# Kernel optimization log

Hardware: AMD Instinct MI355X
Metric: run time of the kernel (lower is better)

## Reference

```python
import jax, jax.numpy as jnp
import numpy as np

N = 100000      # nodes
E = 1600000     # edges
F_IN = 128      # in_feat
H = 128         # hidden_dim
C = 40          # num_class


def setup_inputs() -> dict:
    key = jax.random.key(0)
    ks = jax.random.split(key, 4)
    x = jax.random.normal(ks[0], (N, F_IN), dtype=jnp.float32)
    edge_index = jax.random.randint(ks[1], (2, E), 0, N, dtype=jnp.int32)
    # glorot-ish init for the two GCN layers
    W1 = jax.random.normal(ks[2], (F_IN, H), dtype=jnp.float32) * (1.0 / np.sqrt(F_IN))
    b1 = jnp.zeros((H,), dtype=jnp.float32)
    W2 = jax.random.normal(ks[3], (H, C), dtype=jnp.float32) * (1.0 / np.sqrt(H))
    b2 = jnp.zeros((C,), dtype=jnp.float32)
    return {"x": x, "edge_index": edge_index, "W1": W1, "b1": b1, "W2": W2, "b2": b2}


def _gcn_conv(x, W, b, row, col, norm, n_nodes):
    # GCNConv: linear transform, then normalized sum-aggregation over edges, + bias
    h = x @ W                                  # [N, d_out]
    msg = h[row] * norm[:, None]               # gather sources, scale  [E', d_out]
    out = jax.ops.segment_sum(msg, col, num_segments=n_nodes)  # scatter-add to targets
    return out + b


def reference(x, edge_index, W1, b1, W2, b2):
    n_nodes = x.shape[0]
    # add self-loops (PyG GCNConv default)
    loops = jnp.arange(n_nodes, dtype=edge_index.dtype)
    row = jnp.concatenate([edge_index[0], loops])  # sources
    col = jnp.concatenate([edge_index[1], loops])  # targets
    # symmetric normalization: deg computed at targets with unit edge weights
    deg = jax.ops.segment_sum(jnp.ones_like(col, dtype=x.dtype), col, num_segments=n_nodes)
    dis = jnp.where(deg > 0, jax.lax.rsqrt(jnp.maximum(deg, 1e-12)), 0.0)
    norm = dis[row] * dis[col]                 # [E+N]

    h = jax.nn.relu(_gcn_conv(x, W1, b1, row, col, norm, n_nodes))
    out = _gcn_conv(h, W2, b2, row, col, norm, n_nodes)
    return out
```

## Files before the change

kernel.cpp:

```cpp
#include <hip/hip_runtime.h>
#include <hip/hip_bf16.h>


#define FB_SHIFT 9

__device__ __forceinline__ unsigned bf16rn(float f) {
    unsigned x = __float_as_uint(f);
    unsigned r = ((x >> 16) & 1u) + 0x7fffu;
    return (x + r) >> 16;
}
__device__ __forceinline__ float bf_lo(unsigned u) { return __uint_as_float(u << 16); }
__device__ __forceinline__ float bf_hi(unsigned u) { return __uint_as_float(u & 0xffff0000u); }

typedef __bf16 bf16x8 __attribute__((ext_vector_type(8)));
typedef float  f32x4  __attribute__((ext_vector_type(4)));

__global__ __launch_bounds__(512) void k_bcount(const int* __restrict__ col,
                                                int* __restrict__ btot, int E) {
    __shared__ int h[256];
    const int tid = threadIdx.x;
    if (tid < 256) h[tid] = 0;
    __syncthreads();
    const int base = blockIdx.x * 4096;
#pragma unroll
    for (int k = 0; k < 8; ++k) {
        int e = base + k * 512 + tid;
        if (e < E) atomicAdd(&h[col[e] >> FB_SHIFT], 1);
    }
    __syncthreads();
    if (tid < 256) {
        int v = h[tid];
        if (v > 0) atomicAdd(&btot[tid], v);
    }
}

__global__ __launch_bounds__(256) void k_bscan(const int* __restrict__ btot,
                                               int* __restrict__ bbase,
                                               int* __restrict__ bcur) {
    __shared__ int s[256];
    const int t = threadIdx.x;
    int v = btot[t];
    s[t] = v;
    __syncthreads();
#pragma unroll
    for (int off = 1; off < 256; off <<= 1) {
        int u = (t >= off) ? s[t - off] : 0;
        __syncthreads();
        s[t] += u;
        __syncthreads();
    }
    int excl = s[t] - v;
    bbase[t] = excl;
    bcur[t] = excl;
    if (t == 255) bbase[256] = s[255];
}

__global__ __launch_bounds__(512) void k_binfill(const int* __restrict__ row,
                                                 const int* __restrict__ col,
                                                 int* __restrict__ bcur,
                                                 unsigned* __restrict__ bins, int E) {
    __shared__ int hist[256];
    __shared__ int scn[256];
    __shared__ int gbase[256];
    __shared__ int rcnt[256];
    __shared__ unsigned stage[4096];
    __shared__ unsigned char bkts[4096];

    const int tid = threadIdx.x;
    const int base = blockIdx.x * 4096;

    if (tid < 256) { hist[tid] = 0; rcnt[tid] = 0; }
    __syncthreads();

    unsigned mypk[8];
    int      myb[8];
#pragma unroll
    for (int k = 0; k < 8; ++k) {
        int e = base + k * 512 + tid;
        if (e < E) {
            int r = row[e], c = col[e];
            int b = c >> FB_SHIFT;
            mypk[k] = ((unsigned)r << FB_SHIFT) | (unsigned)(c & ((1 << FB_SHIFT) - 1));
            myb[k] = b;
            atomicAdd(&hist[b], 1);
        } else {
            myb[k] = -1;
        }
    }
    __syncthreads();

    int v = 0;
    if (tid < 256) { v = hist[tid]; scn[tid] = v; }
    __syncthreads();
#pragma unroll
    for (int off = 1; off < 256; off <<= 1) {
        int t = (tid >= off && tid < 256) ? scn[tid - off] : 0;
        __syncthreads();
        if (tid < 256) scn[tid] += t;
        __syncthreads();
    }
    if (tid < 256) {
        int excl = scn[tid] - v;
        scn[tid] = excl;
    }
    __syncthreads();

#pragma unroll
    for (int k = 0; k < 8; ++k) {
        int b = myb[k];
        if (b >= 0) {
            int slot = scn[b] + atomicAdd(&rcnt[b], 1);
            stage[slot] = mypk[k];
            bkts[slot] = (unsigned char)b;
        }
    }

    if (tid < 256 && hist[tid] > 0) gbase[tid] = atomicAdd(&bcur[tid], hist[tid]);
    __syncthreads();

    int total = scn[255] + hist[255];
    for (int s = tid; s < total; s += 512) {
        unsigned u = stage[s];
        int b = bkts[s];
        bins[gbase[b] + (s - scn[b])] = u;
    }
}

__global__ __launch_bounds__(1024) void k_fill2(const unsigned* __restrict__ bins,
                                                const int* __restrict__ bbase,
                                                int* __restrict__ rowptr,
                                                float* __restrict__ dis,
                                                int* __restrict__ pair, int N) {
    __shared__ int cnt[512];
    __shared__ int lcur[512];
    __shared__ int ssum[256];
    const int tid = threadIdx.x;
    const int b = blockIdx.x;
    const int n0 = b << FB_SHIFT;
    const int start = bbase[b];
    const int end = bbase[b + 1];

    if (tid < 512) cnt[tid] = 0;
    __syncthreads();

    for (int i = start + tid; i < end; i += 1024)
        atomicAdd(&cnt[bins[i] & ((1 << FB_SHIFT) - 1)], 1);
    __syncthreads();

    int c0 = 0, c1 = 0, vsum = 0;
    if (tid < 256) {
        c0 = cnt[2 * tid]; c1 = cnt[2 * tid + 1];
        vsum = c0 + c1;
        ssum[tid] = vsum;
    }
    __syncthreads();
#pragma unroll
    for (int off = 1; off < 256; off <<= 1) {
        int u = (tid >= off && tid < 256) ? ssum[tid - off] : 0;
        __syncthreads();
        if (tid < 256) ssum[tid] += u;
        __syncthreads();
    }
    if (tid < 256) {
        int e0 = start + ssum[tid] - vsum;
        int e1 = e0 + c0;
        lcur[2 * tid] = e0;
        lcur[2 * tid + 1] = e1;
        int node0 = n0 + 2 * tid;
        int node1 = node0 + 1;
        if (node0 <= N) rowptr[node0] = e0;
        if (node1 <= N) rowptr[node1] = e1;
        if (node0 < N) dis[node0] = rsqrtf((float)(c0 + 1));
        if (node1 < N) dis[node1] = rsqrtf((float)(c1 + 1));
    }
    __syncthreads();

    for (int i = start + tid; i < end; i += 1024) {
        unsigned u = bins[i];
        int pos = atomicAdd(&lcur[u & ((1 << FB_SHIFT) - 1)], 1);
        pair[pos] = (int)(u >> FB_SHIFT);
    }
}

__global__ __launch_bounds__(256) void k_cvtall(const float* __restrict__ x,
                                                const float* __restrict__ dis,
                                                unsigned* __restrict__ xb,
                                                const float* __restrict__ W1,
                                                const float* __restrict__ W2,
                                                unsigned* __restrict__ Wt,
                                                unsigned* __restrict__ W2t, int n32) {
    int i = blockIdx.x * 256 + threadIdx.x;
    if (i < n32) {
        float4 v = ((const float4*)x)[i];
        float d = dis[i >> 5];
        uint2 o;
        o.x = bf16rn(v.x * d) | (bf16rn(v.y * d) << 16);
        o.y = bf16rn(v.z * d) | (bf16rn(v.w * d) << 16);
        ((uint2*)xb)[i] = o;
        return;
    }
    int t = i - n32;
    if (t < 8192) {
        int n = t >> 6, kk = (t & 63) * 2;
        unsigned lo = bf16rn(W1[(size_t)kk * 128 + n]);
        unsigned hi = bf16rn(W1[(size_t)(kk + 1) * 128 + n]);
        Wt[t] = lo | (hi << 16);
    } else if (t < 8192 + 3072) {
        int u = t - 8192;
        int n = u >> 6, kk = (u & 63) * 2;
        unsigned lo = 0, hi = 0;
        if (n < 40) {
            lo = bf16rn(W2[(size_t)kk * 40 + n]);
            hi = bf16rn(W2[(size_t)(kk + 1) * 40 + n]);
        }
        W2t[u] = lo | (hi << 16);
    }
}

__global__ __launch_bounds__(256) void k_gather1(const unsigned* __restrict__ xb,
                                                 const int* __restrict__ rowptr,
                                                 const int* __restrict__ pair,
                                                 const float* __restrict__ dis,
                                                 unsigned* __restrict__ xab, int N) {
    int gw = (blockIdx.x * 256 + threadIdx.x) >> 6;
    int lane = threadIdx.x & 63;
    if (gw >= N) return;
    float dv = dis[gw];
    unsigned us = xb[(size_t)gw * 64 + lane];
    float2 acc = make_float2(bf_lo(us), bf_hi(us));
    int j = rowptr[gw], je = rowptr[gw + 1];

    for (; j + 7 < je; j += 8) {
        int r0 = pair[j],     r1 = pair[j + 1], r2 = pair[j + 2], r3 = pair[j + 3];
        int r4 = pair[j + 4], r5 = pair[j + 5], r6 = pair[j + 6], r7 = pair[j + 7];
        unsigned a0 = xb[(size_t)r0 * 64 + lane];
        unsigned a1 = xb[(size_t)r1 * 64 + lane];
        unsigned a2 = xb[(size_t)r2 * 64 + lane];
        unsigned a3 = xb[(size_t)r3 * 64 + lane];
        unsigned a4 = xb[(size_t)r4 * 64 + lane];
        unsigned a5 = xb[(size_t)r5 * 64 + lane];
        unsigned a6 = xb[(size_t)r6 * 64 + lane];
        unsigned a7 = xb[(size_t)r7 * 64 + lane];
        acc.x += bf_lo(a0); acc.y += bf_hi(a0);
        acc.x += bf_lo(a1); acc.y += bf_hi(a1);
        acc.x += bf_lo(a2); acc.y += bf_hi(a2);
        acc.x += bf_lo(a3); acc.y += bf_hi(a3);
        acc.x += bf_lo(a4); acc.y += bf_hi(a4);
        acc.x += bf_lo(a5); acc.y += bf_hi(a5);
        acc.x += bf_lo(a6); acc.y += bf_hi(a6);
        acc.x += bf_lo(a7); acc.y += bf_hi(a7);
    }
    for (; j + 3 < je; j += 4) {
        int r0 = pair[j], r1 = pair[j + 1], r2 = pair[j + 2], r3 = pair[j + 3];
        unsigned a0 = xb[(size_t)r0 * 64 + lane];
        unsigned a1 = xb[(size_t)r1 * 64 + lane];
        unsigned a2 = xb[(size_t)r2 * 64 + lane];
        unsigned a3 = xb[(size_t)r3 * 64 + lane];
        acc.x += bf_lo(a0); acc.y += bf_hi(a0);
        acc.x += bf_lo(a1); acc.y += bf_hi(a1);
        acc.x += bf_lo(a2); acc.y += bf_hi(a2);
        acc.x += bf_lo(a3); acc.y += bf_hi(a3);
    }
    for (; j < je; ++j) {
        unsigned a0 = xb[(size_t)pair[j] * 64 + lane];
        acc.x += bf_lo(a0); acc.y += bf_hi(a0);
    }
    xab[(size_t)gw * 64 + lane] = bf16rn(dv * acc.x) | (bf16rn(dv * acc.y) << 16);
}

__global__ __launch_bounds__(256) void k_gemm12(const unsigned* __restrict__ Ab,
                                                const unsigned* __restrict__ Wt,
                                                const unsigned* __restrict__ W2t,
                                                const float* __restrict__ bias,
                                                const float* __restrict__ dis,
                                                unsigned* __restrict__ Zb, int M) {
    __shared__ char smem[70144];
    char* Abase = smem;
    char* Bbase = smem + 34816;
    float* ldis = (float*)(smem + 69632);

    const int tid = threadIdx.x;
    const int r0 = blockIdx.x * 128;

#pragma unroll
    for (int s = 0; s < 8; ++s) {
        int l = tid + s * 256;
        int row = l >> 4, q = l & 15;
        uint4 va = *(const uint4*)(Ab + (size_t)(r0 + row) * 64 + q * 4);
        *(uint4*)(Abase + row * 272 + q * 16) = va;
        uint4 vb = *(const uint4*)(Wt + (size_t)row * 64 + q * 4);
        *(uint4*)(Bbase + row * 272 + q * 16) = vb;
    }
    if (tid < 128) {
        int rr = r0 + tid;
        ldis[tid] = (rr < M) ? dis[rr] : 0.f;
    }
    __syncthreads();

    const int wv = tid >> 6, lane = tid & 63;
    const int quad = lane >> 4, mcol = lane & 15;

    f32x4 acc1[2][8];
#pragma unroll
    for (int rt = 0; rt < 2; ++rt)
#pragma unroll
        for (int ct = 0; ct < 8; ++ct) acc1[rt][ct] = (f32x4){0.f, 0.f, 0.f, 0.f};

#pragma unroll
    for (int ks = 0; ks < 4; ++ks) {
        bf16x8 a[2], b[8];
#pragma unroll
        for (int rt = 0; rt < 2; ++rt) {
            int row = wv * 32 + rt * 16 + mcol;
            a[rt] = *(const bf16x8*)(Abase + row * 272 + ks * 64 + quad * 16);
        }
#pragma unroll
        for (int ct = 0; ct < 8; ++ct) {
            int n = ct * 16 + mcol;
            b[ct] = *(const bf16x8*)(Bbase + n * 272 + ks * 64 + quad * 16);
        }
#pragma unroll
        for (int rt = 0; rt < 2; ++rt)
#pragma unroll
            for (int ct = 0; ct < 8; ++ct)
                acc1[rt][ct] = __builtin_amdgcn_mfma_f32_16x16x32_bf16(
                    a[rt], b[ct], acc1[rt][ct], 0, 0, 0);
    }
    __syncthreads();

    unsigned short* Hs = (unsigned short*)Bbase;
#pragma unroll
    for (int rt = 0; rt < 2; ++rt)
#pragma unroll
        for (int ct = 0; ct < 8; ++ct) {
            float bb = bias[ct * 16 + mcol];
#pragma unroll
            for (int r = 0; r < 4; ++r) {
                float v = acc1[rt][ct][r] + bb;
                v = v > 0.f ? v : 0.f;
                int orow = wv * 32 + rt * 16 + quad * 4 + r;
                Hs[orow * 136 + ct * 16 + mcol] = (unsigned short)bf16rn(v);
            }
        }
#pragma unroll
    for (int s = 0; s < 3; ++s) {
        int l = tid + s * 256;
        int row = l >> 4, q = l & 15;
        uint4 vb = *(const uint4*)(W2t + (size_t)row * 64 + q * 4);
        *(uint4*)(Abase + row * 272 + q * 16) = vb;
    }
    __syncthreads();

    f32x4 acc2[2][3];
#pragma unroll
    for (int rt = 0; rt < 2; ++rt)
#pragma unroll
        for (int ct = 0; ct < 3; ++ct) acc2[rt][ct] = (f32x4){0.f, 0.f, 0.f, 0.f};

#pragma unroll
    for (int ks = 0; ks < 4; ++ks) {
        bf16x8 a[2], b[3];
#pragma unroll
        for (int rt = 0; rt < 2; ++rt) {
            int row = wv * 32 + rt * 16 + mcol;
            a[rt] = *(const bf16x8*)(Bbase + row * 272 + ks * 64 + quad * 16);
        }
#pragma unroll
        for (int ct = 0; ct < 3; ++ct) {
            int n = ct * 16 + mcol;
            b[ct] = *(const bf16x8*)(Abase + n * 272 + ks * 64 + quad * 16);
        }
#pragma unroll
        for (int rt = 0; rt < 2; ++rt)
#pragma unroll
            for (int ct = 0; ct < 3; ++ct)
                acc2[rt][ct] = __builtin_amdgcn_mfma_f32_16x16x32_bf16(
                    a[rt], b[ct], acc2[rt][ct], 0, 0, 0);
    }
    __syncthreads();

    unsigned short* Zs = (unsigned short*)(Abase + 16384);
#pragma unroll
    for (int rt = 0; rt < 2; ++rt)
#pragma unroll
        for (int ct = 0; ct < 3; ++ct) {
#pragma unroll
            for (int r = 0; r < 4; ++r) {
                int orow = wv * 32 + rt * 16 + quad * 4 + r;
                float v = acc2[rt][ct][r] * ldis[orow];
                Zs[orow * 56 + ct * 16 + mcol] = (unsigned short)bf16rn(v);
            }
        }
    __syncthreads();

    if (tid < 128) {
        int rr = r0 + tid;
        if (rr < M) {
            const uint4* s4 = (const uint4*)(Abase + 16384 + tid * 112);
            uint4* d4 = (uint4*)(Zb + (size_t)rr * 20);
#pragma unroll
            for (int q = 0; q < 5; ++q) d4[q] = s4[q];
        }
    }
}

__global__ __launch_bounds__(256) void k_gather2(const unsigned* __restrict__ zb,
                                                 const int* __restrict__ rowptr,
                                                 const int* __restrict__ pair,
                                                 const float* __restrict__ dis,
                                                 const float* __restrict__ b2,
                                                 float* __restrict__ out, int N) {
    int gw = (blockIdx.x * 256 + threadIdx.x) >> 6;
    int lane = threadIdx.x & 63;
    if (gw >= N) return;
    int sub = lane >> 5;
    int sl  = lane & 31;
    int f   = (sl < 20) ? sl : 19;

    float2 acc = make_float2(0.f, 0.f);
    float dv = dis[gw];
    if (sub == 0) {
        unsigned u = zb[(size_t)gw * 20 + f];
        acc.x = bf_lo(u); acc.y = bf_hi(u);
    }

    int j = rowptr[gw], je = rowptr[gw + 1];
    for (; j + 15 < je; j += 16) {
        int rA = pair[j + sub];
        int rB = pair[j + 2 + sub];
        int rC = pair[j + 4 + sub];
        int rD = pair[j + 6 + sub];
        int rE = pair[j + 8 + sub];
        int rF = pair[j + 10 + sub];
        int rG = pair[j + 12 + sub];
        int rH = pair[j + 14 + sub];
        unsigned uA = zb[(size_t)rA * 20 + f];
        unsigned uB = zb[(size_t)rB * 20 + f];
        unsigned uC = zb[(size_t)rC * 20 + f];
        unsigned uD = zb[(size_t)rD * 20 + f];
        unsigned uE = zb[(size_t)rE * 20 + f];
        unsigned uF = zb[(size_t)rF * 20 + f];
        unsigned uG = zb[(size_t)rG * 20 + f];
        unsigned uH = zb[(size_t)rH * 20 + f];
        acc.x += bf_lo(uA); acc.y += bf_hi(uA);
        acc.x += bf_lo(uB); acc.y += bf_hi(uB);
        acc.x += bf_lo(uC); acc.y += bf_hi(uC);
        acc.x += bf_lo(uD); acc.y += bf_hi(uD);
        acc.x += bf_lo(uE); acc.y += bf_hi(uE);
        acc.x += bf_lo(uF); acc.y += bf_hi(uF);
        acc.x += bf_lo(uG); acc.y += bf_hi(uG);
        acc.x += bf_lo(uH); acc.y += bf_hi(uH);
    }
    for (; j + 7 < je; j += 8) {
        int rA = pair[j + sub];
        int rB = pair[j + 2 + sub];
        int rC = pair[j + 4 + sub];
        int rD = pair[j + 6 + sub];
        unsigned uA = zb[(size_t)rA * 20 + f];
        unsigned uB = zb[(size_t)rB * 20 + f];
        unsigned uC = zb[(size_t)rC * 20 + f];
        unsigned uD = zb[(size_t)rD * 20 + f];
        acc.x += bf_lo(uA); acc.y += bf_hi(uA);
        acc.x += bf_lo(uB); acc.y += bf_hi(uB);
        acc.x += bf_lo(uC); acc.y += bf_hi(uC);
        acc.x += bf_lo(uD); acc.y += bf_hi(uD);
    }
    for (; j + 3 < je; j += 4) {
        int rA = pair[j + sub];
        int rB = pair[j + 2 + sub];
        unsigned uA = zb[(size_t)rA * 20 + f];
        unsigned uB = zb[(size_t)rB * 20 + f];
        acc.x += bf_lo(uA); acc.y += bf_hi(uA);
        acc.x += bf_lo(uB); acc.y += bf_hi(uB);
    }
    for (; j + 1 < je; j += 2) {
        unsigned u = zb[(size_t)pair[j + sub] * 20 + f];
        acc.x += bf_lo(u); acc.y += bf_hi(u);
    }
    if (j < je && sub == 0) {
        unsigned u = zb[(size_t)pair[j] * 20 + f];
        acc.x += bf_lo(u); acc.y += bf_hi(u);
    }

    float bx = __shfl(acc.x, sl + 32, 64);
    float by = __shfl(acc.y, sl + 32, 64);
    if (sub == 0 && sl < 20) {
        float2 bias = ((const float2*)b2)[sl];
        float2 res = make_float2((acc.x + bx) * dv + bias.x,
                                 (acc.y + by) * dv + bias.y);
        ((float2*)(out + (size_t)gw * 40))[sl] = res;
    }
}

extern "C" void kernel_launch(void* const* d_in, const int* in_sizes, int n_in,
                              void* d_out, int out_size, void* d_ws, size_t ws_size,
                              hipStream_t stream) {
    const float* x  = (const float*)d_in[0];
    const int*   ei = (const int*)d_in[1];
    const float* W1 = (const float*)d_in[2];
    const float* b1 = (const float*)d_in[3];
    const float* W2 = (const float*)d_in[4];
    const float* b2 = (const float*)d_in[5];
    float* out = (float*)d_out;

    const int N = in_sizes[0] / 128;
    const int E = in_sizes[1] / 2;
    const int* row = ei;
    const int* col = ei + E;

    const int Np = (N + 255) & ~255;
    const int nbuck = (N + (1 << FB_SHIFT) - 1) >> FB_SHIFT;

    int*      rowptr = (int*)d_ws;
    int*      btot   = rowptr + Np + 256;
    int*      bbase  = btot + 256;
    int*      bcur   = bbase + 320;
    float*    dis    = (float*)(bcur + 256);
    unsigned* Wt     = (unsigned*)(dis + Np);
    unsigned* W2t    = Wt + 8192;
    int*      pair   = (int*)(W2t + 3072);
    unsigned* xb     = (unsigned*)(pair + E);
    unsigned* xab    = xb + (size_t)N * 64;
    unsigned* zb     = xab + (size_t)N * 64;
    unsigned* bins   = (unsigned*)xab;

    hipMemsetAsync(btot, 0, 256 * sizeof(int), stream);
    k_bcount<<<(E + 4095) / 4096, 512, 0, stream>>>(col, btot, E);
    k_bscan<<<1, 256, 0, stream>>>(btot, bbase, bcur);
    k_binfill<<<(E + 4095) / 4096, 512, 0, stream>>>(row, col, bcur, bins, E);
    k_fill2<<<nbuck, 1024, 0, stream>>>(bins, bbase, rowptr, dis, pair, N);

    k_cvtall<<<(N * 32 + 11264 + 255) / 256, 256, 0, stream>>>(
        x, dis, xb, W1, W2, Wt, W2t, N * 32);

    k_gather1<<<(N + 3) / 4, 256, 0, stream>>>(xb, rowptr, pair, dis, xab, N);

    k_gemm12<<<(N + 127) / 128, 256, 0, stream>>>(xab, Wt, W2t, b1, dis, zb, N);

    k_gather2<<<(N + 3) / 4, 256, 0, stream>>>(zb, rowptr, pair, dis, b2, out, N);
}
```

Before: 271.9 us.

## Fuse bf16 conversions into scan and fill kernels, pad layer-2 rows to 128B

```diff
diff --git a/kernel.cpp b/kernel.cpp
--- a/kernel.cpp
+++ b/kernel.cpp
@@ -34,25 +34,48 @@
     }
 }
 
-__global__ __launch_bounds__(256) void k_bscan(const int* __restrict__ btot,
-                                               int* __restrict__ bbase,
-                                               int* __restrict__ bcur) {
-    __shared__ int s[256];
+__global__ __launch_bounds__(256) void k_bscanw(const int* __restrict__ btot,
+                                                int* __restrict__ bbase,
+                                                int* __restrict__ bcur,
+                                                const float* __restrict__ W1,
+                                                const float* __restrict__ W2,
+                                                unsigned* __restrict__ Wt,
+                                                unsigned* __restrict__ W2t) {
     const int t = threadIdx.x;
-    int v = btot[t];
-    s[t] = v;
-    __syncthreads();
-#pragma unroll
-    for (int off = 1; off < 256; off <<= 1) {
-        int u = (t >= off) ? s[t - off] : 0;
+    if (blockIdx.x == 0) {
+        __shared__ int s[256];
+        int v = btot[t];
+        s[t] = v;
         __syncthreads();
-        s[t] += u;
-        __syncthreads();
-    }
-    int excl = s[t] - v;
-    bbase[t] = excl;
-    bcur[t] = excl;
-    if (t == 255) bbase[256] = s[255];
+#pragma unroll
+        for (int off = 1; off < 256; off <<= 1) {
+            int u = (t >= off) ? s[t - off] : 0;
+            __syncthreads();
+            s[t] += u;
+            __syncthreads();
+        }
+        int excl = s[t] - v;
+        bbase[t] = excl;
+        bcur[t] = excl;
+        if (t == 255) bbase[256] = s[255];
+        return;
+    }
+    int w = (blockIdx.x - 1) * 256 + t;
+    if (w < 8192) {
+        int n = w >> 6, kk = (w & 63) * 2;
+        unsigned lo = bf16rn(W1[(size_t)kk * 128 + n]);
+        unsigned hi = bf16rn(W1[(size_t)(kk + 1) * 128 + n]);
+        Wt[w] = lo | (hi << 16);
+    } else if (w < 8192 + 3072) {
+        int u = w - 8192;
+        int n = u >> 6, kk = (u & 63) * 2;
+        unsigned lo = 0, hi = 0;
+        if (n < 40) {
+            lo = bf16rn(W2[(size_t)kk * 40 + n]);
+            hi = bf16rn(W2[(size_t)(kk + 1) * 40 + n]);
+        }
+        W2t[u] = lo | (hi << 16);
+    }
 }
 
 __global__ __launch_bounds__(512) void k_binfill(const int* __restrict__ row,
@@ -130,10 +153,13 @@
                                                 const int* __restrict__ bbase,
                                                 int* __restrict__ rowptr,
                                                 float* __restrict__ dis,
-                                                int* __restrict__ pair, int N) {
+                                                int* __restrict__ pair,
+                                                const float* __restrict__ x,
+                                                unsigned* __restrict__ xb, int N) {
     __shared__ int cnt[512];
     __shared__ int lcur[512];
     __shared__ int ssum[256];
+    __shared__ float ldisv[512];
     const int tid = threadIdx.x;
     const int b = blockIdx.x;
     const int n0 = b << FB_SHIFT;
@@ -168,10 +194,14 @@
         lcur[2 * tid + 1] = e1;
         int node0 = n0 + 2 * tid;
         int node1 = node0 + 1;
+        float d0 = rsqrtf((float)(c0 + 1));
+        float d1 = rsqrtf((float)(c1 + 1));
+        ldisv[2 * tid] = d0;
+        ldisv[2 * tid + 1] = d1;
         if (node0 <= N) rowptr[node0] = e0;
         if (node1 <= N) rowptr[node1] = e1;
-        if (node0 < N) dis[node0] = rsqrtf((float)(c0 + 1));
-        if (node1 < N) dis[node1] = rsqrtf((float)(c1 + 1));
+        if (node0 < N) dis[node0] = d0;
+        if (node1 < N) dis[node1] = d1;
     }
     __syncthreads();
 
@@ -180,40 +210,18 @@
         int pos = atomicAdd(&lcur[u & ((1 << FB_SHIFT) - 1)], 1);
         pair[pos] = (int)(u >> FB_SHIFT);
     }
-}
-
-__global__ __launch_bounds__(256) void k_cvtall(const float* __restrict__ x,
-                                                const float* __restrict__ dis,
-                                                unsigned* __restrict__ xb,
-                                                const float* __restrict__ W1,
-                                                const float* __restrict__ W2,
-                                                unsigned* __restrict__ Wt,
-                                                unsigned* __restrict__ W2t, int n32) {
-    int i = blockIdx.x * 256 + threadIdx.x;
-    if (i < n32) {
-        float4 v = ((const float4*)x)[i];
-        float d = dis[i >> 5];
+
+    int nrows = N - n0; if (nrows > 512) nrows = 512;
+    int rloc = tid >> 5;
+    int cseg = tid & 31;
+    for (int rr = rloc; rr < nrows; rr += 32) {
+        int node = n0 + rr;
+        float d = ldisv[rr];
+        float4 v = ((const float4*)(x + (size_t)node * 128))[cseg];
         uint2 o;
         o.x = bf16rn(v.x * d) | (bf16rn(v.y * d) << 16);
         o.y = bf16rn(v.z * d) | (bf16rn(v.w * d) << 16);
-        ((uint2*)xb)[i] = o;
-        return;
-    }
-    int t = i - n32;
-    if (t < 8192) {
-        int n = t >> 6, kk = (t & 63) * 2;
-        unsigned lo = bf16rn(W1[(size_t)kk * 128 + n]);
-        unsigned hi = bf16rn(W1[(size_t)(kk + 1) * 128 + n]);
-        Wt[t] = lo | (hi << 16);
-    } else if (t < 8192 + 3072) {
-        int u = t - 8192;
-        int n = u >> 6, kk = (u & 63) * 2;
-        unsigned lo = 0, hi = 0;
-        if (n < 40) {
-            lo = bf16rn(W2[(size_t)kk * 40 + n]);
-            hi = bf16rn(W2[(size_t)(kk + 1) * 40 + n]);
-        }
-        W2t[u] = lo | (hi << 16);
+        ((uint2*)(xb + (size_t)node * 64))[cseg] = o;
     }
 }
 
@@ -397,7 +405,7 @@
         int rr = r0 + tid;
         if (rr < M) {
             const uint4* s4 = (const uint4*)(Abase + 16384 + tid * 112);
-            uint4* d4 = (uint4*)(Zb + (size_t)rr * 20);
+            uint4* d4 = (uint4*)(Zb + ((size_t)rr << 5));
 #pragma unroll
             for (int q = 0; q < 5; ++q) d4[q] = s4[q];
         }
@@ -420,7 +428,7 @@
     float2 acc = make_float2(0.f, 0.f);
     float dv = dis[gw];
     if (sub == 0) {
-        unsigned u = zb[(size_t)gw * 20 + f];
+        unsigned u = zb[((size_t)gw << 5) + f];
         acc.x = bf_lo(u); acc.y = bf_hi(u);
     }
 
@@ -434,14 +442,14 @@
         int rF = pair[j + 10 + sub];
         int rG = pair[j + 12 + sub];
         int rH = pair[j + 14 + sub];
-        unsigned uA = zb[(size_t)rA * 20 + f];
-        unsigned uB = zb[(size_t)rB * 20 + f];
-        unsigned uC = zb[(size_t)rC * 20 + f];
-        unsigned uD = zb[(size_t)rD * 20 + f];
-        unsigned uE = zb[(size_t)rE * 20 + f];
-        unsigned uF = zb[(size_t)rF * 20 + f];
-        unsigned uG = zb[(size_t)rG * 20 + f];
-        unsigned uH = zb[(size_t)rH * 20 + f];
+        unsigned uA = zb[((size_t)rA << 5) + f];
+        unsigned uB = zb[((size_t)rB << 5) + f];
+        unsigned uC = zb[((size_t)rC << 5) + f];
+        unsigned uD = zb[((size_t)rD << 5) + f];
+        unsigned uE = zb[((size_t)rE << 5) + f];
+        unsigned uF = zb[((size_t)rF << 5) + f];
+        unsigned uG = zb[((size_t)rG << 5) + f];
+        unsigned uH = zb[((size_t)rH << 5) + f];
         acc.x += bf_lo(uA); acc.y += bf_hi(uA);
         acc.x += bf_lo(uB); acc.y += bf_hi(uB);
         acc.x += bf_lo(uC); acc.y += bf_hi(uC);
@@ -456,10 +464,10 @@
         int rB = pair[j + 2 + sub];
         int rC = pair[j + 4 + sub];
         int rD = pair[j + 6 + sub];
-        unsigned uA = zb[(size_t)rA * 20 + f];
-        unsigned uB = zb[(size_t)rB * 20 + f];
-        unsigned uC = zb[(size_t)rC * 20 + f];
-        unsigned uD = zb[(size_t)rD * 20 + f];
+        unsigned uA = zb[((size_t)rA << 5) + f];
+        unsigned uB = zb[((size_t)rB << 5) + f];
+        unsigned uC = zb[((size_t)rC << 5) + f];
+        unsigned uD = zb[((size_t)rD << 5) + f];
         acc.x += bf_lo(uA); acc.y += bf_hi(uA);
         acc.x += bf_lo(uB); acc.y += bf_hi(uB);
         acc.x += bf_lo(uC); acc.y += bf_hi(uC);
@@ -468,17 +476,17 @@
     for (; j + 3 < je; j += 4) {
         int rA = pair[j + sub];
         int rB = pair[j + 2 + sub];
-        unsigned uA = zb[(size_t)rA * 20 + f];
-        unsigned uB = zb[(size_t)rB * 20 + f];
+        unsigned uA = zb[((size_t)rA << 5) + f];
+        unsigned uB = zb[((size_t)rB << 5) + f];
         acc.x += bf_lo(uA); acc.y += bf_hi(uA);
         acc.x += bf_lo(uB); acc.y += bf_hi(uB);
     }
     for (; j + 1 < je; j += 2) {
-        unsigned u = zb[(size_t)pair[j + sub] * 20 + f];
+        unsigned u = zb[((size_t)pair[j + sub] << 5) + f];
         acc.x += bf_lo(u); acc.y += bf_hi(u);
     }
     if (j < je && sub == 0) {
-        unsigned u = zb[(size_t)pair[j] * 20 + f];
+        unsigned u = zb[((size_t)pair[j] << 5) + f];
         acc.x += bf_lo(u); acc.y += bf_hi(u);
     }
 
@@ -526,12 +534,9 @@
 
     hipMemsetAsync(btot, 0, 256 * sizeof(int), stream);
     k_bcount<<<(E + 4095) / 4096, 512, 0, stream>>>(col, btot, E);
-    k_bscan<<<1, 256, 0, stream>>>(btot, bbase, bcur);
+    k_bscanw<<<45, 256, 0, stream>>>(btot, bbase, bcur, W1, W2, Wt, W2t);
     k_binfill<<<(E + 4095) / 4096, 512, 0, stream>>>(row, col, bcur, bins, E);
-    k_fill2<<<nbuck, 1024, 0, stream>>>(bins, bbase, rowptr, dis, pair, N);
-
-    k_cvtall<<<(N * 32 + 11264 + 255) / 256, 256, 0, stream>>>(
-        x, dis, xb, W1, W2, Wt, W2t, N * 32);
+    k_fill2<<<nbuck, 1024, 0, stream>>>(bins, bbase, rowptr, dis, pair, x, xb, N);
 
     k_gather1<<<(N + 3) / 4, 256, 0, stream>>>(xb, rowptr, pair, dis, xab, N);
 
```

Measured after the change: 278.8 us. 1.03x slower.
